# Performance work log

Hardware: AMD Instinct MI355X
Metric: run time of the kernel (lower is better)

Reference implementation:

```python
import jax, jax.numpy as jnp
import numpy as np

EPS = 1e-5  # BatchNorm1d default eps


def _xavier_uniform(key, shape):
    # torch xavier: fan_in = shape[1]*prod(shape[2:]), fan_out = shape[0]*prod(shape[2:])
    rf = int(np.prod(shape[2:])) if len(shape) > 2 else 1
    fan_in = shape[1] * rf
    fan_out = shape[0] * rf
    bound = float(np.sqrt(6.0 / (fan_in + fan_out)))
    return jax.random.uniform(key, shape, jnp.float32, -bound, bound)


def setup_inputs() -> dict:
    key = jax.random.key(0)
    ks = jax.random.split(key, 6)
    d_in, h1, h2, d_out = 256, 512, 512, 256
    B = 4096
    x = jax.random.normal(ks[0], (B, 1, d_in), dtype=jnp.float32)
    W1 = _xavier_uniform(ks[1], (h1, d_in))
    b1 = jnp.zeros((h1,), jnp.float32)
    gamma = jnp.ones((1, 1, 1), jnp.float32)   # BatchNorm1d(1) weight
    beta = jnp.zeros((1, 1, 1), jnp.float32)   # BatchNorm1d(1) bias
    coeffs2 = _xavier_uniform(ks[2], (2, h2, h1, 16))
    bias2 = jnp.zeros((1, h2), jnp.float32)
    coeffs3 = _xavier_uniform(ks[3], (2, d_out, h2, 8))
    bias3 = jnp.zeros((1, d_out), jnp.float32)
    return {"x": x, "W1": W1, "b1": b1, "gamma": gamma, "beta": beta,
            "coeffs2": coeffs2, "bias2": bias2, "coeffs3": coeffs3, "bias3": bias3}


def _fourier_kan(x, coeffs, bias, gridsize):
    # x: (N, in)  coeffs: (2, out, in, grid)  ->  (N, out)
    k = jnp.arange(1, gridsize + 1, dtype=x.dtype)          # (grid,)
    arg = x[:, :, None] * k                                  # (N, in, grid) -- basis computed ONCE
    y = jnp.einsum('nig,oig->no', jnp.cos(arg), coeffs[0])
    y = y + jnp.einsum('nig,oig->no', jnp.sin(arg), coeffs[1])
    return y + bias


def reference(x, W1, b1, gamma, beta, coeffs2, bias2, coeffs3, bias3):
    # x: (B, 1, d_in)
    h = jnp.einsum('bcd,hd->bch', x, W1) + b1                # Linear -> (B,1,h1)
    # BatchNorm1d(1), training-mode batch stats over (N, L) for the single channel
    mean = jnp.mean(h, axis=(0, 2), keepdims=True)
    var = jnp.mean((h - mean) ** 2, axis=(0, 2), keepdims=True)
    h = gamma * (h - mean) * jax.lax.rsqrt(var + EPS) + beta
    h = jax.nn.relu(h)
    h = h.reshape(-1, h.shape[-1])                           # (B, h1)
    h = _fourier_kan(h, coeffs2, bias2, 16)                  # (B, h2)
    h = _fourier_kan(h, coeffs3, bias3, 8)                   # (B, out)
    return jax.nn.softmax(h, axis=1)
```

## Files before the change

### kernel.cpp

```cpp
#include <hip/hip_runtime.h>
#include <hip/hip_fp16.h>
#include <stdint.h>

typedef unsigned short u16;
typedef unsigned int u32;
typedef long i64;
typedef short bf16x8 __attribute__((ext_vector_type(8)));
typedef float f32x4 __attribute__((ext_vector_type(4)));

#define SCALE_C   1024.f
#define INV_SCALE 0.0009765625f

__device__ __forceinline__ float bf2f(u16 v) { return __uint_as_float(((u32)v) << 16); }

__device__ __forceinline__ u16 f2bf(float a) {
  u32 u = __float_as_uint(a); u += 0x7FFFu + ((u >> 16) & 1u); return (u16)(u >> 16);
}

__device__ __forceinline__ u32 packbf2(float a, float b) {
  u32 ua = __float_as_uint(a); ua += 0x7FFFu + ((ua >> 16) & 1u);
  u32 ub = __float_as_uint(b); ub += 0x7FFFu + ((ub >> 16) & 1u);
  return (ua >> 16) | (ub & 0xFFFF0000u);
}

__device__ __forceinline__ u32 packfp8x4(float a, float b, float c, float d) {
  u32 lo = (u32)__builtin_amdgcn_cvt_pk_fp8_f32(a, b, 0, false);
  return (u32)__builtin_amdgcn_cvt_pk_fp8_f32(c, d, (int)lo, true);
}

__device__ __forceinline__ float inval(const void* p, int idx, int isf) {
  return isf ? ((const float*)p)[idx] : bf2f(((const u16*)p)[idx]);
}

__device__ __forceinline__ void async_cp16(const void* g, void* l) {
  __builtin_amdgcn_global_load_lds(
      (const __attribute__((address_space(1))) void*)g,
      (__attribute__((address_space(3))) void*)l, 16, 0, 0);
}

__device__ __forceinline__ void basis16(float a, u32* pk) {
  float s1, c1; __sincosf(a, &s1, &c1);
  float t2 = c1 + c1;
  float cg[16], sg[16];
  cg[0] = c1; sg[0] = s1;
  cg[1] = fmaf(t2, c1, -1.f); sg[1] = t2 * s1;
  #pragma unroll
  for (int g = 2; g < 16; ++g) {
    cg[g] = fmaf(t2, cg[g-1], -cg[g-2]);
    sg[g] = fmaf(t2, sg[g-1], -sg[g-2]);
  }
  #pragma unroll
  for (int j = 0; j < 4; ++j) pk[j]   = packfp8x4(cg[4*j], cg[4*j+1], cg[4*j+2], cg[4*j+3]);
  #pragma unroll
  for (int j = 0; j < 4; ++j) pk[4+j] = packfp8x4(sg[4*j], sg[4*j+1], sg[4*j+2], sg[4*j+3]);
}

__device__ __forceinline__ void split_body(
    const void* __restrict__ src, u16* __restrict__ dst, int i, int isf, int lo_pos)
{
  int row = i >> 6, g = i & 63;
  float v[4];
  if (isf) {
    float4 t = ((const float4*)src)[i];
    v[0] = t.x; v[1] = t.y; v[2] = t.z; v[3] = t.w;
  } else {
    uint2 t = ((const uint2*)src)[i];
    const u16* p = (const u16*)&t;
    v[0] = bf2f(p[0]); v[1] = bf2f(p[1]); v[2] = bf2f(p[2]); v[3] = bf2f(p[3]);
  }
  u16 hi[4]; float lo[4];
  #pragma unroll
  for (int j = 0; j < 4; ++j) { hi[j] = f2bf(v[j]); lo[j] = v[j] - bf2f(hi[j]); }
  u32 hw0 = (u32)hi[0] | ((u32)hi[1] << 16);
  u32 hw1 = (u32)hi[2] | ((u32)hi[3] << 16);
  u32 lw0 = packbf2(lo[0], lo[1]);
  u32 lw1 = packbf2(lo[2], lo[3]);
  u32* base = (u32*)(dst + (size_t)row * 768);
  int c = g * 2;
  base[c] = hw0; base[c + 1] = hw1;
  if (lo_pos == 1) {
    base[128 + c] = lw0; base[128 + c + 1] = lw1;
    base[256 + c] = hw0; base[256 + c + 1] = hw1;
  } else {
    base[128 + c] = hw0; base[128 + c + 1] = hw1;
    base[256 + c] = lw0; base[256 + c + 1] = lw1;
  }
}

__global__ __launch_bounds__(256) void prep_all_kernel(
    const void* __restrict__ x, const void* __restrict__ W1,
    u16* __restrict__ Xs, u16* __restrict__ W1s,
    const void* __restrict__ c2, unsigned char* __restrict__ w2f8,
    const void* __restrict__ c3, unsigned char* __restrict__ w3f8,
    int* __restrict__ flag)
{
  __shared__ int sf[4];
  const int t = threadIdx.x, wave = t >> 6;
  {
    float v = fabsf(bf2f(((const u16*)W1)[t & 127]));
    int bad = !(v < 1e6f);
    unsigned long long b = __ballot(bad);
    if ((t & 63) == 0) sf[wave] = (b != 0ull) ? 1 : 0;
  }
  __syncthreads();
  const int isf = sf[0] | sf[1] | sf[2] | sf[3];
  const int bid = blockIdx.x;
  if (bid == 0 && t == 0) *flag = isf;
  if (bid < 1024) {
    split_body(x, Xs, bid * 256 + t, isf, 1);
  } else if (bid < 1152) {
    split_body(W1, W1s, (bid - 1024) * 256 + t, isf, 2);
  } else if (bid < 2176) {
    int u = (bid - 1152) * 256 + t;
    int o = u >> 9, i = u & 511;
    u32* d = (u32*)(w2f8 + (size_t)o * 16384 + i * 32);
    if (isf) {
      const float4* f0 = (const float4*)((const float*)c2 + ((size_t)o * 512 + i) * 16);
      const float4* f1 = (const float4*)((const float*)c2 + (size_t)512 * 512 * 16 + ((size_t)o * 512 + i) * 16);
      #pragma unroll
      for (int j = 0; j < 4; ++j) { float4 v = f0[j]; d[j]   = packfp8x4(v.x*SCALE_C, v.y*SCALE_C, v.z*SCALE_C, v.w*SCALE_C); }
      #pragma unroll
      for (int j = 0; j < 4; ++j) { float4 v = f1[j]; d[4+j] = packfp8x4(v.x*SCALE_C, v.y*SCALE_C, v.z*SCALE_C, v.w*SCALE_C); }
    } else {
      const u16* s0 = (const u16*)c2 + ((size_t)o * 512 + i) * 16;
      const u16* s1 = (const u16*)c2 + (size_t)512 * 512 * 16 + ((size_t)o * 512 + i) * 16;
      #pragma unroll
      for (int j = 0; j < 4; ++j) d[j]   = packfp8x4(bf2f(s0[4*j])*SCALE_C, bf2f(s0[4*j+1])*SCALE_C, bf2f(s0[4*j+2])*SCALE_C, bf2f(s0[4*j+3])*SCALE_C);
      #pragma unroll
      for (int j = 0; j < 4; ++j) d[4+j] = packfp8x4(bf2f(s1[4*j])*SCALE_C, bf2f(s1[4*j+1])*SCALE_C, bf2f(s1[4*j+2])*SCALE_C, bf2f(s1[4*j+3])*SCALE_C);
    }
  } else {
    int u = (bid - 2176) * 256 + t;
    int o = u >> 9, i = u & 511;
    u32* d = (u32*)(w3f8 + (size_t)o * 8192 + i * 16);
    if (isf) {
      const float4* f0 = (const float4*)((const float*)c3 + ((size_t)o * 512 + i) * 8);
      const float4* f1 = (const float4*)((const float*)c3 + (size_t)256 * 512 * 8 + ((size_t)o * 512 + i) * 8);
      #pragma unroll
      for (int j = 0; j < 2; ++j) { float4 v = f0[j]; d[j]   = packfp8x4(v.x*SCALE_C, v.y*SCALE_C, v.z*SCALE_C, v.w*SCALE_C); }
      #pragma unroll
      for (int j = 0; j < 2; ++j) { float4 v = f1[j]; d[2+j] = packfp8x4(v.x*SCALE_C, v.y*SCALE_C, v.z*SCALE_C, v.w*SCALE_C); }
    } else {
      const u16* s0 = (const u16*)c3 + ((size_t)o * 512 + i) * 8;
      const u16* s1 = (const u16*)c3 + (size_t)256 * 512 * 8 + ((size_t)o * 512 + i) * 8;
      #pragma unroll
      for (int j = 0; j < 2; ++j) d[j]   = packfp8x4(bf2f(s0[4*j])*SCALE_C, bf2f(s0[4*j+1])*SCALE_C, bf2f(s0[4*j+2])*SCALE_C, bf2f(s0[4*j+3])*SCALE_C);
      #pragma unroll
      for (int j = 0; j < 2; ++j) d[2+j] = packfp8x4(bf2f(s1[4*j])*SCALE_C, bf2f(s1[4*j+1])*SCALE_C, bf2f(s1[4*j+2])*SCALE_C, bf2f(s1[4*j+3])*SCALE_C);
    }
  }
}

#define L1_LD 136
__global__ __launch_bounds__(256) void l1_kernel(
    const u16* __restrict__ xs, const u16* __restrict__ w1s, const void* __restrict__ b1,
    const int* __restrict__ flag, float* __restrict__ H, float2* __restrict__ PT)
{
  __shared__ u16 sA[64 * L1_LD];
  __shared__ u16 sB[64 * L1_LD];
  __shared__ float redbuf[8];
  const int n0 = blockIdx.x * 64, o0 = blockIdx.y * 64;
  const int t = threadIdx.x, wave = t >> 6, lane = t & 63, quad = lane >> 4, l16 = lane & 15;
  const int isf = *flag;
  f32x4 acc[4] = {};
  for (int ks = 0; ks < 768; ks += 128) {
    #pragma unroll
    for (int r = 0; r < 4; ++r) {
      int idx = t + r * 256, row = idx >> 4, col = idx & 15;
      *(uint4*)&sA[row * L1_LD + col * 8] =
          *((const uint4*)(xs + (size_t)(n0 + row) * 768 + ks) + col);
    }
    #pragma unroll
    for (int r = 0; r < 4; ++r) {
      int idx = t + r * 256, row = idx >> 4, col = idx & 15;
      *(uint4*)&sB[row * L1_LD + col * 8] =
          *((const uint4*)(w1s + (size_t)(o0 + row) * 768 + ks) + col);
    }
    __syncthreads();
    #pragma unroll
    for (int kk = 0; kk < 128; kk += 32) {
      bf16x8 av = *(const bf16x8*)&sA[(wave * 16 + l16) * L1_LD + kk + quad * 8];
      #pragma unroll
      for (int fo = 0; fo < 4; ++fo) {
        bf16x8 bv = *(const bf16x8*)&sB[(fo * 16 + l16) * L1_LD + kk + quad * 8];
        acc[fo] = __builtin_amdgcn_mfma_f32_16x16x32_bf16(av, bv, acc[fo], 0, 0, 0);
      }
    }
    __syncthreads();
  }
  float s = 0.f, sq = 0.f;
  #pragma unroll
  for (int fo = 0; fo < 4; ++fo) {
    int o = o0 + fo * 16 + l16;
    float bias = inval(b1, o, isf);
    #pragma unroll
    for (int r = 0; r < 4; ++r) {
      int n = n0 + wave * 16 + quad * 4 + r;
      float h = acc[fo][r] + bias;
      H[(size_t)n * 512 + o] = h;
      s += h; sq += h * h;
    }
  }
  #pragma unroll
  for (int off = 32; off; off >>= 1) { s += __shfl_down(s, off); sq += __shfl_down(sq, off); }
  if (lane == 0) { redbuf[wave] = s; redbuf[4 + wave] = sq; }
  __syncthreads();
  if (t == 0) {
    float S = redbuf[0] + redbuf[1] + redbuf[2] + redbuf[3];
    float Q = redbuf[4] + redbuf[5] + redbuf[6] + redbuf[7];
    PT[blockIdx.y * 64 + blockIdx.x] = make_float2(S, Q);
  }
}

#define K2_LDB 128
__global__ __launch_bounds__(512, 4) void kan2_kernel(
    const float* __restrict__ H, const unsigned char* __restrict__ w2f8,
    const void* __restrict__ gammap, const void* __restrict__ betap,
    const int* __restrict__ flag, const float2* __restrict__ PT,
    float* __restrict__ P, int kzT)
{
  __shared__ __attribute__((aligned(16))) unsigned char smem[81920];
  float* sred = (float*)(smem + 81888);
  const int n0 = blockIdx.x * 64, o0 = blockIdx.y * 256, kz = blockIdx.z;
  const int t = threadIdx.x, wave = t >> 6, lane = t & 63, quad = lane >> 4, l16 = lane & 15;
  const int nst = 128 / kzT;
  const int i0 = kz * nst * 4;
  const int csw = (l16 & 7) << 4;
  const int isf = *flag;

  const int pt = t - 256;
  const int am = pt >> 2, ai = pt & 3;
  const int r0 = pt >> 3, seg = pt & 7;
  const unsigned char* bsrc = w2f8 + (size_t)(o0 + (r0 & 63)) * 16384 + (size_t)i0 * 32
                              + (((seg & 7) * 16) ^ ((r0 & 7) << 4));
  const float* hsrc = H + (size_t)(n0 + (am & 63)) * 512 + i0 + (ai & 3);
  const int acol0 = ((ai & 3) * 32) ^ ((am & 7) << 4);
  const int acol1 = ((ai & 3) * 32 + 16) ^ ((am & 7) << 4);
  float mean = 0.f, gs = 0.f, beta = 0.f, ph = 0.f;
  u32 pk[8];

  if (wave >= 4) {
    unsigned char* b0 = smem + 16384 + (wave - 4) * 1024;
    #pragma unroll
    for (int p = 0; p < 8; ++p)
      async_cp16(bsrc + (size_t)p * 32 * 16384, b0 + p * 4096);
    float2 pa = PT[pt], pb = PT[pt + 256];
    float ss = pa.x + pb.x, qs = pa.y + pb.y;
    #pragma unroll
    for (int off = 32; off; off >>= 1) { ss += __shfl_down(ss, off); qs += __shfl_down(qs, off); }
    if (lane == 0) { sred[(wave - 4) * 2] = ss; sred[(wave - 4) * 2 + 1] = qs; }
  }
  __syncthreads();
  if (wave >= 4) {
    const float Ssum = sred[0] + sred[2] + sred[4] + sred[6];
    const float Qsum = sred[1] + sred[3] + sred[5] + sred[7];
    const float Nn = 4096.f * 512.f;
    mean = Ssum / Nn;
    const float rstd = rsqrtf(Qsum / Nn - mean * mean + 1e-5f);
    gs = inval(gammap, 0, isf) * rstd;
    beta = inval(betap, 0, isf);
    float a = fmaxf((*hsrc - mean) * gs + beta, 0.f);
    hsrc += 4;
    basis16(a, pk);
    *(uint4*)&smem[am * K2_LDB + acol0] = *(uint4*)&pk[0];
    *(uint4*)&smem[am * K2_LDB + acol1] = *(uint4*)&pk[4];
    if (nst > 1) { ph = *hsrc; hsrc += 4; }
  }
  __syncthreads();

  f32x4 acc[2][8] = {};
  const int wm = (wave & 1) * 32, wo = (wave >> 1) * 128;
  int cur = 0;
  for (int s = 0; s < nst; ++s) {
    const int nxt = cur ^ 1;
    if (wave >= 4) {
      if (s + 1 < nst) {
        bsrc += 128;
        unsigned char* bn = smem + 16384 + nxt * 32768 + (wave - 4) * 1024;
        #pragma unroll
        for (int p = 0; p < 8; ++p)
          async_cp16(bsrc + (size_t)p * 32 * 16384, bn + p * 4096);
        float a = fmaxf((ph - mean) * gs + beta, 0.f);
        basis16(a, pk);
        unsigned char* an = smem + nxt * 8192;
        *(uint4*)&an[am * K2_LDB + acol0] = *(uint4*)&pk[0];
        *(uint4*)&an[am * K2_LDB + acol1] = *(uint4*)&pk[4];
        if (s + 2 < nst) { ph = *hsrc; hsrc += 4; }
      }
    } else {
      const unsigned char* ac = smem + cur * 8192;
      const unsigned char* bc = smem + 16384 + cur * 32768;
      #pragma unroll
      for (int kk = 0; kk < 128; kk += 32) {
        const int cb = (kk + quad * 8) ^ csw;
        i64 bfr[8], afr[2];
        #pragma unroll
        for (int fo = 0; fo < 8; ++fo)
          bfr[fo] = *(const i64*)&bc[(wo + fo * 16 + l16) * K2_LDB + cb];
        #pragma unroll
        for (int fm = 0; fm < 2; ++fm)
          afr[fm] = *(const i64*)&ac[(wm + fm * 16 + l16) * K2_LDB + cb];
        #pragma unroll
        for (int fm = 0; fm < 2; ++fm)
        #pragma unroll
        for (int fo = 0; fo < 8; ++fo)
          acc[fm][fo] = __builtin_amdgcn_mfma_f32_16x16x32_fp8_fp8(afr[fm], bfr[fo], acc[fm][fo], 0, 0, 0);
      }
    }
    __syncthreads();
    cur = nxt;
  }
  if (wave < 4) {
    float* Pk = P + (size_t)kz * (4096 * 512);
    #pragma unroll
    for (int fm = 0; fm < 2; ++fm)
    #pragma unroll
    for (int fo = 0; fo < 8; ++fo) {
      int o = o0 + wo + fo * 16 + l16;
      #pragma unroll
      for (int r = 0; r < 4; ++r) {
        int n = n0 + wm + fm * 16 + quad * 4 + r;
        Pk[(size_t)n * 512 + o] = acc[fm][fo][r] * INV_SCALE;
      }
    }
  }
}

#define K3_LDB 128
__global__ __launch_bounds__(256) void kan3_kernel(
    const float* __restrict__ P2, const void* __restrict__ bias2,
    const unsigned char* __restrict__ w3f8,
    const int* __restrict__ flag, float* __restrict__ Q, int kzT2)
{
  __shared__ unsigned char sA8[32 * K3_LDB];
  __shared__ unsigned char sB8[256 * K3_LDB];
  const int n0 = blockIdx.x * 32, kz = blockIdx.z;
  const int t = threadIdx.x, wave = t >> 6, lane = t & 63, quad = lane >> 4, l16 = lane & 15;
  const int wo = wave * 64;
  const int am = t >> 3, ai = t & 7;
  const int nst = 10 + (kz < 4 ? 1 : 0);
  const int i0 = (kz * 10 + (kz < 4 ? kz : 4)) * 8;
  const int r0 = t >> 3, seg = t & 7;
  const int isf = *flag;
  const unsigned char* bsrc = w3f8 + (size_t)r0 * 8192 + (size_t)i0 * 16
                              + ((seg * 16) ^ ((r0 & 7) << 4));
  const float* psrc = P2 + (size_t)(n0 + am) * 512 + i0 + ai;
  unsigned char* ldsB = &sB8[wave * 8 * K3_LDB];
  const int acol = (ai * 16) ^ ((am & 7) << 4);
  const int csw  = (l16 & 7) << 4;
  f32x4 acc[2][4] = {};
  #pragma unroll
  for (int p = 0; p < 8; ++p)
    async_cp16(bsrc + (size_t)p * 32 * 8192, ldsB + p * 32 * K3_LDB);
  float ph;
  {
    float v = inval(bias2, i0 + ai, isf);
    for (int k = 0; k < kzT2; ++k) v += psrc[(size_t)k * 4096 * 512];
    ph = v;
  }
  for (int s = 0; s < nst; ++s) {
    {
      float s1, c1; __sincosf(ph, &s1, &c1);
      float t2 = c1 + c1;
      float cg[8], sg[8];
      cg[0] = c1; sg[0] = s1;
      cg[1] = fmaf(t2, c1, -1.f); sg[1] = t2 * s1;
      #pragma unroll
      for (int g = 2; g < 8; ++g) {
        cg[g] = fmaf(t2, cg[g-1], -cg[g-2]);
        sg[g] = fmaf(t2, sg[g-1], -sg[g-2]);
      }
      u32 pk[4];
      pk[0] = packfp8x4(cg[0], cg[1], cg[2], cg[3]);
      pk[1] = packfp8x4(cg[4], cg[5], cg[6], cg[7]);
      pk[2] = packfp8x4(sg[0], sg[1], sg[2], sg[3]);
      pk[3] = packfp8x4(sg[4], sg[5], sg[6], sg[7]);
      *(uint4*)&sA8[am * K3_LDB + acol] = *(uint4*)&pk[0];
    }
    __syncthreads();
    psrc += 8;
    if (s + 1 < nst) {
      float v = inval(bias2, i0 + (s + 1) * 8 + ai, isf);
      for (int k = 0; k < kzT2; ++k) v += psrc[(size_t)k * 4096 * 512];
      ph = v;
    }
    #pragma unroll
    for (int kk = 0; kk < 128; kk += 32) {
      const int cb = (kk + quad * 8) ^ csw;
      i64 bfr[4], afr[2];
      #pragma unroll
      for (int fo = 0; fo < 4; ++fo)
        bfr[fo] = *(const i64*)&sB8[(wo + fo * 16 + l16) * K3_LDB + cb];
      #pragma unroll
      for (int fm = 0; fm < 2; ++fm)
        afr[fm] = *(const i64*)&sA8[(fm * 16 + l16) * K3_LDB + cb];
      #pragma unroll
      for (int fm = 0; fm < 2; ++fm)
      #pragma unroll
      for (int fo = 0; fo < 4; ++fo)
        acc[fm][fo] = __builtin_amdgcn_mfma_f32_16x16x32_fp8_fp8(afr[fm], bfr[fo], acc[fm][fo], 0, 0, 0);
    }
    __syncthreads();
    bsrc += 128;
    if (s + 1 < nst) {
      #pragma unroll
      for (int p = 0; p < 8; ++p)
        async_cp16(bsrc + (size_t)p * 32 * 8192, ldsB + p * 32 * K3_LDB);
    }
  }
  float* Qk = Q + (size_t)kz * (4096 * 256);
  #pragma unroll
  for (int fm = 0; fm < 2; ++fm)
  #pragma unroll
  for (int fo = 0; fo < 4; ++fo) {
    int o = wo + fo * 16 + l16;
    #pragma unroll
    for (int r = 0; r < 4; ++r) {
      int n = n0 + fm * 16 + quad * 4 + r;
      Qk[(size_t)n * 256 + o] = acc[fm][fo][r] * INV_SCALE;
    }
  }
}

__global__ __launch_bounds__(256) void softmax_kernel(
    const float* __restrict__ Q, const void* __restrict__ bias3,
    const int* __restrict__ flag, float* __restrict__ out)
{
  const int t = threadIdx.x, wave = t >> 6, lane = t & 63;
  const int row = blockIdx.x * 4 + wave;
  const int isf = *flag;
  size_t base = (size_t)row * 256 + lane * 4;
  float v0 = 0.f, v1 = 0.f, v2 = 0.f, v3 = 0.f;
  #pragma unroll
  for (int k = 0; k < 6; ++k) {
    float4 a = *(const float4*)(Q + (size_t)k * 4096 * 256 + base);
    v0 += a.x; v1 += a.y; v2 += a.z; v3 += a.w;
  }
  int o = lane * 4;
  v0 += inval(bias3, o + 0, isf);
  v1 += inval(bias3, o + 1, isf);
  v2 += inval(bias3, o + 2, isf);
  v3 += inval(bias3, o + 3, isf);
  float m = fmaxf(fmaxf(v0, v1), fmaxf(v2, v3));
  #pragma unroll
  for (int off = 32; off; off >>= 1) m = fmaxf(m, __shfl_xor(m, off));
  float e0 = __expf(v0 - m), e1 = __expf(v1 - m), e2 = __expf(v2 - m), e3 = __expf(v3 - m);
  float s = e0 + e1 + e2 + e3;
  #pragma unroll
  for (int off = 32; off; off >>= 1) s += __shfl_xor(s, off);
  float inv = 1.f / s;
  *(float4*)(out + base) = make_float4(e0 * inv, e1 * inv, e2 * inv, e3 * inv);
}

extern "C" void kernel_launch(void* const* d_in, const int* in_sizes, int n_in,
                              void* d_out, int out_size, void* d_ws, size_t ws_size,
                              hipStream_t stream)
{
  const void* x     = d_in[0];
  const void* W1    = d_in[1];
  const void* b1    = d_in[2];
  const void* gamma = d_in[3];
  const void* beta  = d_in[4];
  const void* c2    = d_in[5];
  const void* bias2 = d_in[6];
  const void* c3    = d_in[7];
  const void* bias3 = d_in[8];

  const int kz2 = 4;

  char* ws = (char*)d_ws;
  float*          H    = (float*)(ws + 0);
  unsigned char*  W2F8 = (unsigned char*)(ws + (16ull << 20));
  unsigned char*  W3F8 = (unsigned char*)(ws + (24ull << 20));
  u16*            Xs   = (u16*)(ws + (26ull << 20));
  u16*            W1s  = (u16*)(ws + (33ull << 20));
  float*          P2   = (float*)(ws + (34ull << 20));
  float*          Q3   = (float*)(ws + 0);
  size_t tail = (34ull << 20) + (size_t)kz2 * (8ull << 20) + 524288;
  float2* PT   = (float2*)(ws + tail);
  int*    FLAG = (int*)   (ws + tail + 65536);

  prep_all_kernel<<<dim3(2688), dim3(256), 0, stream>>>(x, W1, Xs, W1s, c2, W2F8, c3, W3F8, FLAG);
  l1_kernel   <<<dim3(64, 8), dim3(256), 0, stream>>>(Xs, W1s, b1, FLAG, H, PT);
  kan2_kernel <<<dim3(64, 2, kz2), dim3(512), 0, stream>>>(H, W2F8, gamma, beta, FLAG, PT, P2, kz2);
  kan3_kernel <<<dim3(128, 1, 6), dim3(256), 0, stream>>>(P2, bias2, W3F8, FLAG, Q3, kz2);
  softmax_kernel<<<dim3(1024), dim3(256), 0, stream>>>(Q3, bias3, FLAG, (float*)d_out);
}
```

Before: 198.7 us.

## Reshape kan2 block tile to 128 rows by 128 outputs

The kan2 block tile changes from 64 batch rows × 256 outputs to 128 × 128, and the grid becomes 32×4×kz. Each producer thread now computes two Fourier basis values per step (float2 load of H), and each consumer wave covers 32 rows × all 128 outputs. This halves the FP8 weight traffic staged per step and doubles the basis work per block. The aim is a better balance between recomputing the basis and loading weights, plus lower LDS use (64KB). The exchange is that the basis for each H row is recomputed across 4 output blocks instead of 2.

```diff
diff --git a/kernel.cpp b/kernel.cpp
--- a/kernel.cpp
+++ b/kernel.cpp
@@ -219,9 +219,9 @@
     const int* __restrict__ flag, const float2* __restrict__ PT,
     float* __restrict__ P, int kzT)
 {
-  __shared__ __attribute__((aligned(16))) unsigned char smem[81920];
-  float* sred = (float*)(smem + 81888);
-  const int n0 = blockIdx.x * 64, o0 = blockIdx.y * 256, kz = blockIdx.z;
+  __shared__ __attribute__((aligned(16))) unsigned char smem[65536];
+  __shared__ float sred[8];
+  const int n0 = blockIdx.x * 128, o0 = blockIdx.y * 128, kz = blockIdx.z;
   const int t = threadIdx.x, wave = t >> 6, lane = t & 63, quad = lane >> 4, l16 = lane & 15;
   const int nst = 128 / kzT;
   const int i0 = kz * nst * 4;
@@ -229,20 +229,21 @@
   const int isf = *flag;
 
   const int pt = t - 256;
-  const int am = pt >> 2, ai = pt & 3;
-  const int r0 = pt >> 3, seg = pt & 7;
-  const unsigned char* bsrc = w2f8 + (size_t)(o0 + (r0 & 63)) * 16384 + (size_t)i0 * 32
-                              + (((seg & 7) * 16) ^ ((r0 & 7) << 4));
-  const float* hsrc = H + (size_t)(n0 + (am & 63)) * 512 + i0 + (ai & 3);
-  const int acol0 = ((ai & 3) * 32) ^ ((am & 7) << 4);
-  const int acol1 = ((ai & 3) * 32 + 16) ^ ((am & 7) << 4);
-  float mean = 0.f, gs = 0.f, beta = 0.f, ph = 0.f;
-  u32 pk[8];
+  const int am = (pt >> 1) & 127;
+  const int ib = (pt & 1) * 2;
+  const int r0 = (pt >> 3) & 31, seg = pt & 7;
+  const unsigned char* bsrc = w2f8 + (size_t)(o0 + r0) * 16384 + (size_t)i0 * 32
+                              + ((seg * 16) ^ ((r0 & 7) << 4));
+  const float* hsrc = H + (size_t)(n0 + am) * 512 + i0 + ib;
+  const int asw = (am & 7) << 4;
+  float mean = 0.f, gs = 0.f, beta = 0.f;
+  float2 ph2 = make_float2(0.f, 0.f);
+  u32 pk0[8], pk1[8];
 
   if (wave >= 4) {
-    unsigned char* b0 = smem + 16384 + (wave - 4) * 1024;
-    #pragma unroll
-    for (int p = 0; p < 8; ++p)
+    unsigned char* b0 = smem + 32768 + (wave - 4) * 1024;
+    #pragma unroll
+    for (int p = 0; p < 4; ++p)
       async_cp16(bsrc + (size_t)p * 32 * 16384, b0 + p * 4096);
     float2 pa = PT[pt], pb = PT[pt + 256];
     float ss = pa.x + pb.x, qs = pa.y + pb.y;
@@ -259,44 +260,52 @@
     const float rstd = rsqrtf(Qsum / Nn - mean * mean + 1e-5f);
     gs = inval(gammap, 0, isf) * rstd;
     beta = inval(betap, 0, isf);
-    float a = fmaxf((*hsrc - mean) * gs + beta, 0.f);
-    hsrc += 4;
-    basis16(a, pk);
-    *(uint4*)&smem[am * K2_LDB + acol0] = *(uint4*)&pk[0];
-    *(uint4*)&smem[am * K2_LDB + acol1] = *(uint4*)&pk[4];
-    if (nst > 1) { ph = *hsrc; hsrc += 4; }
+    ph2 = *(const float2*)hsrc; hsrc += 4;
+    float a0 = fmaxf((ph2.x - mean) * gs + beta, 0.f);
+    float a1 = fmaxf((ph2.y - mean) * gs + beta, 0.f);
+    basis16(a0, pk0);
+    basis16(a1, pk1);
+    *(uint4*)&smem[am * K2_LDB + ((ib * 32) ^ asw)]           = *(uint4*)&pk0[0];
+    *(uint4*)&smem[am * K2_LDB + ((ib * 32 + 16) ^ asw)]      = *(uint4*)&pk0[4];
+    *(uint4*)&smem[am * K2_LDB + (((ib + 1) * 32) ^ asw)]     = *(uint4*)&pk1[0];
+    *(uint4*)&smem[am * K2_LDB + (((ib + 1) * 32 + 16) ^ asw)] = *(uint4*)&pk1[4];
+    if (nst > 1) { ph2 = *(const float2*)hsrc; hsrc += 4; }
   }
   __syncthreads();
 
   f32x4 acc[2][8] = {};
-  const int wm = (wave & 1) * 32, wo = (wave >> 1) * 128;
+  const int wm = wave * 32;
   int cur = 0;
   for (int s = 0; s < nst; ++s) {
     const int nxt = cur ^ 1;
     if (wave >= 4) {
       if (s + 1 < nst) {
         bsrc += 128;
-        unsigned char* bn = smem + 16384 + nxt * 32768 + (wave - 4) * 1024;
+        unsigned char* bn = smem + 32768 + nxt * 16384 + (wave - 4) * 1024;
         #pragma unroll
-        for (int p = 0; p < 8; ++p)
+        for (int p = 0; p < 4; ++p)
           async_cp16(bsrc + (size_t)p * 32 * 16384, bn + p * 4096);
-        float a = fmaxf((ph - mean) * gs + beta, 0.f);
-        basis16(a, pk);
-        unsigned char* an = smem + nxt * 8192;
-        *(uint4*)&an[am * K2_LDB + acol0] = *(uint4*)&pk[0];
-        *(uint4*)&an[am * K2_LDB + acol1] = *(uint4*)&pk[4];
-        if (s + 2 < nst) { ph = *hsrc; hsrc += 4; }
+        float a0 = fmaxf((ph2.x - mean) * gs + beta, 0.f);
+        float a1 = fmaxf((ph2.y - mean) * gs + beta, 0.f);
+        basis16(a0, pk0);
+        basis16(a1, pk1);
+        unsigned char* an = smem + nxt * 16384;
+        *(uint4*)&an[am * K2_LDB + ((ib * 32) ^ asw)]            = *(uint4*)&pk0[0];
+        *(uint4*)&an[am * K2_LDB + ((ib * 32 + 16) ^ asw)]       = *(uint4*)&pk0[4];
+        *(uint4*)&an[am * K2_LDB + (((ib + 1) * 32) ^ asw)]      = *(uint4*)&pk1[0];
+        *(uint4*)&an[am * K2_LDB + (((ib + 1) * 32 + 16) ^ asw)] = *(uint4*)&pk1[4];
+        if (s + 2 < nst) { ph2 = *(const float2*)hsrc; hsrc += 4; }
       }
     } else {
-      const unsigned char* ac = smem + cur * 8192;
-      const unsigned char* bc = smem + 16384 + cur * 32768;
+      const unsigned char* ac = smem + cur * 16384;
+      const unsigned char* bc = smem + 32768 + cur * 16384;
       #pragma unroll
       for (int kk = 0; kk < 128; kk += 32) {
         const int cb = (kk + quad * 8) ^ csw;
         i64 bfr[8], afr[2];
         #pragma unroll
         for (int fo = 0; fo < 8; ++fo)
-          bfr[fo] = *(const i64*)&bc[(wo + fo * 16 + l16) * K2_LDB + cb];
+          bfr[fo] = *(const i64*)&bc[(fo * 16 + l16) * K2_LDB + cb];
         #pragma unroll
         for (int fm = 0; fm < 2; ++fm)
           afr[fm] = *(const i64*)&ac[(wm + fm * 16 + l16) * K2_LDB + cb];
@@ -316,7 +325,7 @@
     for (int fm = 0; fm < 2; ++fm)
     #pragma unroll
     for (int fo = 0; fo < 8; ++fo) {
-      int o = o0 + wo + fo * 16 + l16;
+      int o = o0 + fo * 16 + l16;
       #pragma unroll
       for (int r = 0; r < 4; ++r) {
         int n = n0 + wm + fm * 16 + quad * 4 + r;
@@ -482,7 +491,7 @@
 
   prep_all_kernel<<<dim3(2688), dim3(256), 0, stream>>>(x, W1, Xs, W1s, c2, W2F8, c3, W3F8, FLAG);
   l1_kernel   <<<dim3(64, 8), dim3(256), 0, stream>>>(Xs, W1s, b1, FLAG, H, PT);
-  kan2_kernel <<<dim3(64, 2, kz2), dim3(512), 0, stream>>>(H, W2F8, gamma, beta, FLAG, PT, P2, kz2);
+  kan2_kernel <<<dim3(32, 4, kz2), dim3(512), 0, stream>>>(H, W2F8, gamma, beta, FLAG, PT, P2, kz2);
   kan3_kernel <<<dim3(128, 1, 6), dim3(256), 0, stream>>>(P2, bias2, W3F8, FLAG, Q3, kz2);
   softmax_kernel<<<dim3(1024), dim3(256), 0, stream>>>(Q3, bias3, FLAG, (float*)d_out);
 }
```

Result: no change. 200.2 us (+0.7%).

## Warp-specialize KAN3 kernel with producer waves and double-buffered LDS

Applied to the files above, without the earlier changes.

The layer-3 Fourier-KAN kernel now uses 512 threads. Four producer waves compute the basis and issue async weight copies into a double-buffered LDS stage, while four consumer waves run the FP8 MFMAs at raised priority. The row tile grows from 32 to 64 rows and the split-K goes from 6 to 8 slices, with the partial outputs placed at scattered workspace offsets that the softmax kernel now sums. This aims to overlap the sin/cos basis generation and weight loads with the matrix math. The cost is roughly 80 KB of LDS per block and one more partial buffer to read in softmax.

```diff
diff --git a/kernel.cpp b/kernel.cpp
--- a/kernel.cpp
+++ b/kernel.cpp
@@ -54,6 +54,25 @@
   #pragma unroll
   for (int j = 0; j < 4; ++j) pk[4+j] = packfp8x4(sg[4*j], sg[4*j+1], sg[4*j+2], sg[4*j+3]);
 }
+
+__device__ __forceinline__ void basis8(float a, u32* pk) {
+  float s1, c1; __sincosf(a, &s1, &c1);
+  float t2 = c1 + c1;
+  float cg[8], sg[8];
+  cg[0] = c1; sg[0] = s1;
+  cg[1] = fmaf(t2, c1, -1.f); sg[1] = t2 * s1;
+  #pragma unroll
+  for (int g = 2; g < 8; ++g) {
+    cg[g] = fmaf(t2, cg[g-1], -cg[g-2]);
+    sg[g] = fmaf(t2, sg[g-1], -sg[g-2]);
+  }
+  pk[0] = packfp8x4(cg[0], cg[1], cg[2], cg[3]);
+  pk[1] = packfp8x4(cg[4], cg[5], cg[6], cg[7]);
+  pk[2] = packfp8x4(sg[0], sg[1], sg[2], sg[3]);
+  pk[3] = packfp8x4(sg[4], sg[5], sg[6], sg[7]);
+}
+
+#define QOF(k) ((size_t)((k) < 6 ? (k) * 4 : 26 + ((k) - 6) * 4) << 20)
 
 __device__ __forceinline__ void split_body(
     const void* __restrict__ src, u16* __restrict__ dst, int i, int isf, int lo_pos)
@@ -327,103 +346,126 @@
 }
 
 #define K3_LDB 128
-__global__ __launch_bounds__(256) void kan3_kernel(
+__global__ __launch_bounds__(512, 4) void kan3_kernel(
     const float* __restrict__ P2, const void* __restrict__ bias2,
     const unsigned char* __restrict__ w3f8,
-    const int* __restrict__ flag, float* __restrict__ Q, int kzT2)
-{
-  __shared__ unsigned char sA8[32 * K3_LDB];
-  __shared__ unsigned char sB8[256 * K3_LDB];
-  const int n0 = blockIdx.x * 32, kz = blockIdx.z;
+    const int* __restrict__ flag, char* __restrict__ wsbase, int kzT2)
+{
+  __shared__ __attribute__((aligned(16))) unsigned char smem[81920];
+  const int n0 = blockIdx.x * 64, kz = blockIdx.z;
   const int t = threadIdx.x, wave = t >> 6, lane = t & 63, quad = lane >> 4, l16 = lane & 15;
-  const int wo = wave * 64;
-  const int am = t >> 3, ai = t & 7;
-  const int nst = 10 + (kz < 4 ? 1 : 0);
-  const int i0 = (kz * 10 + (kz < 4 ? kz : 4)) * 8;
-  const int r0 = t >> 3, seg = t & 7;
+  const int i0 = kz * 64;
+  const int nst = 8;
+  const int csw = (l16 & 7) << 4;
   const int isf = *flag;
+
+  const int pt = t - 256;
+  const int am = (pt >> 2) & 63;
+  const int il = (pt & 3) * 2;
+  const int r0 = (pt >> 3) & 31, seg = pt & 7;
   const unsigned char* bsrc = w3f8 + (size_t)r0 * 8192 + (size_t)i0 * 16
                               + ((seg * 16) ^ ((r0 & 7) << 4));
-  const float* psrc = P2 + (size_t)(n0 + am) * 512 + i0 + ai;
-  unsigned char* ldsB = &sB8[wave * 8 * K3_LDB];
-  const int acol = (ai * 16) ^ ((am & 7) << 4);
-  const int csw  = (l16 & 7) << 4;
-  f32x4 acc[2][4] = {};
-  #pragma unroll
-  for (int p = 0; p < 8; ++p)
-    async_cp16(bsrc + (size_t)p * 32 * 8192, ldsB + p * 32 * K3_LDB);
-  float ph;
-  {
-    float v = inval(bias2, i0 + ai, isf);
-    for (int k = 0; k < kzT2; ++k) v += psrc[(size_t)k * 4096 * 512];
-    ph = v;
-  }
+  const float* psrc = P2 + (size_t)(n0 + am) * 512 + i0 + il;
+  const int acol0 = (il * 16) ^ ((am & 7) << 4);
+  const int acol1 = ((il + 1) * 16) ^ ((am & 7) << 4);
+  float2 ph2 = make_float2(0.f, 0.f);
+  u32 pkA[4], pkB[4];
+
+  if (wave >= 4) {
+    unsigned char* b0 = smem + 16384 + (wave - 4) * 1024;
+    #pragma unroll
+    for (int p = 0; p < 8; ++p)
+      async_cp16(bsrc + (size_t)p * 32 * 8192, b0 + p * 4096);
+    float v0 = inval(bias2, i0 + il, isf);
+    float v1 = inval(bias2, i0 + il + 1, isf);
+    for (int k = 0; k < kzT2; ++k) {
+      float2 pp = *(const float2*)(psrc + (size_t)k * 4096 * 512);
+      v0 += pp.x; v1 += pp.y;
+    }
+    basis8(v0, pkA); basis8(v1, pkB);
+    *(uint4*)&smem[am * K3_LDB + acol0] = *(uint4*)&pkA[0];
+    *(uint4*)&smem[am * K3_LDB + acol1] = *(uint4*)&pkB[0];
+    psrc += 8;
+    float w0 = inval(bias2, i0 + 8 + il, isf);
+    float w1 = inval(bias2, i0 + 8 + il + 1, isf);
+    for (int k = 0; k < kzT2; ++k) {
+      float2 pp = *(const float2*)(psrc + (size_t)k * 4096 * 512);
+      w0 += pp.x; w1 += pp.y;
+    }
+    ph2 = make_float2(w0, w1);
+  }
+  __syncthreads();
+
+  f32x4 acc[4][4] = {};
+  const int wo = wave * 64;
+  int cur = 0;
   for (int s = 0; s < nst; ++s) {
-    {
-      float s1, c1; __sincosf(ph, &s1, &c1);
-      float t2 = c1 + c1;
-      float cg[8], sg[8];
-      cg[0] = c1; sg[0] = s1;
-      cg[1] = fmaf(t2, c1, -1.f); sg[1] = t2 * s1;
-      #pragma unroll
-      for (int g = 2; g < 8; ++g) {
-        cg[g] = fmaf(t2, cg[g-1], -cg[g-2]);
-        sg[g] = fmaf(t2, sg[g-1], -sg[g-2]);
-      }
-      u32 pk[4];
-      pk[0] = packfp8x4(cg[0], cg[1], cg[2], cg[3]);
-      pk[1] = packfp8x4(cg[4], cg[5], cg[6], cg[7]);
-      pk[2] = packfp8x4(sg[0], sg[1], sg[2], sg[3]);
-      pk[3] = packfp8x4(sg[4], sg[5], sg[6], sg[7]);
-      *(uint4*)&sA8[am * K3_LDB + acol] = *(uint4*)&pk[0];
+    const int nxt = cur ^ 1;
+    if (wave >= 4) {
+      if (s + 1 < nst) {
+        bsrc += 128;
+        unsigned char* bn = smem + 16384 + nxt * 32768 + (wave - 4) * 1024;
+        #pragma unroll
+        for (int p = 0; p < 8; ++p)
+          async_cp16(bsrc + (size_t)p * 32 * 8192, bn + p * 4096);
+        basis8(ph2.x, pkA); basis8(ph2.y, pkB);
+        unsigned char* an = smem + nxt * 8192;
+        *(uint4*)&an[am * K3_LDB + acol0] = *(uint4*)&pkA[0];
+        *(uint4*)&an[am * K3_LDB + acol1] = *(uint4*)&pkB[0];
+        if (s + 2 < nst) {
+          psrc += 8;
+          float w0 = inval(bias2, i0 + (s + 2) * 8 + il, isf);
+          float w1 = inval(bias2, i0 + (s + 2) * 8 + il + 1, isf);
+          for (int k = 0; k < kzT2; ++k) {
+            float2 pp = *(const float2*)(psrc + (size_t)k * 4096 * 512);
+            w0 += pp.x; w1 += pp.y;
+          }
+          ph2 = make_float2(w0, w1);
+        }
+      }
+    } else {
+      const unsigned char* ac = smem + cur * 8192;
+      const unsigned char* bc = smem + 16384 + cur * 32768;
+      __builtin_amdgcn_s_setprio(1);
+      #pragma unroll
+      for (int kk = 0; kk < 128; kk += 32) {
+        const int cb = (kk + quad * 8) ^ csw;
+        i64 bfr[4], afr[4];
+        #pragma unroll
+        for (int fo = 0; fo < 4; ++fo)
+          bfr[fo] = *(const i64*)&bc[(wo + fo * 16 + l16) * K3_LDB + cb];
+        #pragma unroll
+        for (int fm = 0; fm < 4; ++fm)
+          afr[fm] = *(const i64*)&ac[(fm * 16 + l16) * K3_LDB + cb];
+        #pragma unroll
+        for (int fm = 0; fm < 4; ++fm)
+        #pragma unroll
+        for (int fo = 0; fo < 4; ++fo)
+          acc[fm][fo] = __builtin_amdgcn_mfma_f32_16x16x32_fp8_fp8(afr[fm], bfr[fo], acc[fm][fo], 0, 0, 0);
+      }
+      __builtin_amdgcn_s_setprio(0);
     }
     __syncthreads();
-    psrc += 8;
-    if (s + 1 < nst) {
-      float v = inval(bias2, i0 + (s + 1) * 8 + ai, isf);
-      for (int k = 0; k < kzT2; ++k) v += psrc[(size_t)k * 4096 * 512];
-      ph = v;
-    }
-    #pragma unroll
-    for (int kk = 0; kk < 128; kk += 32) {
-      const int cb = (kk + quad * 8) ^ csw;
-      i64 bfr[4], afr[2];
-      #pragma unroll
-      for (int fo = 0; fo < 4; ++fo)
-        bfr[fo] = *(const i64*)&sB8[(wo + fo * 16 + l16) * K3_LDB + cb];
-      #pragma unroll
-      for (int fm = 0; fm < 2; ++fm)
-        afr[fm] = *(const i64*)&sA8[(fm * 16 + l16) * K3_LDB + cb];
-      #pragma unroll
-      for (int fm = 0; fm < 2; ++fm)
-      #pragma unroll
-      for (int fo = 0; fo < 4; ++fo)
-        acc[fm][fo] = __builtin_amdgcn_mfma_f32_16x16x32_fp8_fp8(afr[fm], bfr[fo], acc[fm][fo], 0, 0, 0);
-    }
-    __syncthreads();
-    bsrc += 128;
-    if (s + 1 < nst) {
-      #pragma unroll
-      for (int p = 0; p < 8; ++p)
-        async_cp16(bsrc + (size_t)p * 32 * 8192, ldsB + p * 32 * K3_LDB);
-    }
-  }
-  float* Qk = Q + (size_t)kz * (4096 * 256);
-  #pragma unroll
-  for (int fm = 0; fm < 2; ++fm)
-  #pragma unroll
-  for (int fo = 0; fo < 4; ++fo) {
-    int o = wo + fo * 16 + l16;
-    #pragma unroll
-    for (int r = 0; r < 4; ++r) {
-      int n = n0 + fm * 16 + quad * 4 + r;
-      Qk[(size_t)n * 256 + o] = acc[fm][fo][r] * INV_SCALE;
+    cur = nxt;
+  }
+  if (wave < 4) {
+    float* Qk = (float*)(wsbase + QOF(kz));
+    #pragma unroll
+    for (int fm = 0; fm < 4; ++fm)
+    #pragma unroll
+    for (int fo = 0; fo < 4; ++fo) {
+      int o = wo + fo * 16 + l16;
+      #pragma unroll
+      for (int r = 0; r < 4; ++r) {
+        int n = n0 + fm * 16 + quad * 4 + r;
+        Qk[(size_t)n * 256 + o] = acc[fm][fo][r] * INV_SCALE;
+      }
     }
   }
 }
 
 __global__ __launch_bounds__(256) void softmax_kernel(
-    const float* __restrict__ Q, const void* __restrict__ bias3,
+    const char* __restrict__ wsbase, const void* __restrict__ bias3,
     const int* __restrict__ flag, float* __restrict__ out)
 {
   const int t = threadIdx.x, wave = t >> 6, lane = t & 63;
@@ -432,8 +474,8 @@
   size_t base = (size_t)row * 256 + lane * 4;
   float v0 = 0.f, v1 = 0.f, v2 = 0.f, v3 = 0.f;
   #pragma unroll
-  for (int k = 0; k < 6; ++k) {
-    float4 a = *(const float4*)(Q + (size_t)k * 4096 * 256 + base);
+  for (int k = 0; k < 8; ++k) {
+    float4 a = *(const float4*)((const float*)(wsbase + QOF(k)) + base);
     v0 += a.x; v1 += a.y; v2 += a.z; v3 += a.w;
   }
   int o = lane * 4;
@@ -475,7 +517,6 @@
   u16*            Xs   = (u16*)(ws + (26ull << 20));
   u16*            W1s  = (u16*)(ws + (33ull << 20));
   float*          P2   = (float*)(ws + (34ull << 20));
-  float*          Q3   = (float*)(ws + 0);
   size_t tail = (34ull << 20) + (size_t)kz2 * (8ull << 20) + 524288;
   float2* PT   = (float2*)(ws + tail);
   int*    FLAG = (int*)   (ws + tail + 65536);
@@ -483,6 +524,6 @@
   prep_all_kernel<<<dim3(2688), dim3(256), 0, stream>>>(x, W1, Xs, W1s, c2, W2F8, c3, W3F8, FLAG);
   l1_kernel   <<<dim3(64, 8), dim3(256), 0, stream>>>(Xs, W1s, b1, FLAG, H, PT);
   kan2_kernel <<<dim3(64, 2, kz2), dim3(512), 0, stream>>>(H, W2F8, gamma, beta, FLAG, PT, P2, kz2);
-  kan3_kernel <<<dim3(128, 1, 6), dim3(256), 0, stream>>>(P2, bias2, W3F8, FLAG, Q3, kz2);
-  softmax_kernel<<<dim3(1024), dim3(256), 0, stream>>>(Q3, bias3, FLAG, (float*)d_out);
-}
+  kan3_kernel <<<dim3(64, 1, 8), dim3(512), 0, stream>>>(P2, bias2, W3F8, FLAG, ws, kz2);
+  softmax_kernel<<<dim3(1024), dim3(256), 0, stream>>>(ws, bias3, FLAG, (float*)d_out);
+}
```

After: 195.2 us. About the same (-1.8%).
